# Performance work log

Measured on AMD Instinct MI355X. Metric: run time of the kernel, lower is better.

## Reference

```python
import jax, jax.numpy as jnp
import numpy as np

LS = (0, 2, 4, 6, 8)
L_IN, L_OUT, SYM = 8, 8, 2
A, B, N, C = 2, 2, 1024, 8  # ti_n, te_n, voxels, b_out

def _triples():
    out = []
    for l in range(0, L_OUT + 1, SYM):
        for l1 in range(0, L_IN + 1, SYM):
            for l2 in range(l1, L_IN + 1, SYM):
                if abs(l2 - l1) <= l <= l1 + l2:
                    out.append((l, l1, l2))
    return tuple(out)

TRIPLES = _triples()
# Clebsch-Gordan-like constants (fixed random; same structural shapes as the real CG tables)
_rng = np.random.RandomState(42)
CG_R = {t: jnp.asarray((_rng.randn(2 * t[0] + 1, 2 * t[1] + 1, 2 * t[2] + 1) * 0.1).astype(np.float32)) for t in TRIPLES}
CG_L = {t: jnp.asarray((_rng.randn(2 * t[0] + 1, 2 * t[2] + 1, 2 * t[1] + 1) * 0.1).astype(np.float32)) for t in TRIPLES}


def setup_inputs() -> dict:
    key = jax.random.key(0)
    ks = jax.random.split(key, 11)
    inp = {}
    for i, l in enumerate(LS):
        i_l = 5 if l == 0 else 2
        inp[f"x{l}"] = jax.random.normal(ks[i], (A, B, N, i_l, 2 * l + 1), dtype=jnp.float32)
        inp[f"w{l}"] = jax.random.uniform(ks[5 + i], (A, B, i_l, C, 2 * l + 1), dtype=jnp.float32) * 0.1
    inp["bias"] = jnp.zeros((A, B, 1, C, 1, 1), dtype=jnp.float32)
    return inp


def _forward(x0, x2, x4, x6, x8, w0, w2, w4, w6, w8, bias):
    xs = {0: x0, 2: x2, 4: x4, 6: x6, 8: x8}
    ws = {0: w0, 2: w2, 4: w4, 6: w6, 8: w8}
    # spectral convolution: rh[l] = x[l] @ w[l], shape (a,b,n,c,2l+1,2l+1)
    rh = {}
    for l in LS:
        r = jnp.einsum('abnil,abiok->abnolk', xs[l], ws[l])
        if l == 0:
            r = r + bias
        rh[l] = r
    # CG tensor-product quadratic nonlinearity
    rh_n = {}
    for (l, l1, l2) in TRIPLES:
        a, b, n, c = rh[l1].shape[:4]
        xx = jnp.einsum('abncij,klj->abnckli', rh[l2], CG_R[(l, l1, l2)])
        xx = xx.reshape(a, b, n, c, 2 * l + 1, -1)  # flat dim = (2l1+1)*(2l2+1)
        yy = jnp.einsum('abncji,klj->abnckil', rh[l1], CG_L[(l, l1, l2)])
        yy = yy.reshape(a, b, n, c, 2 * l + 1, -1)
        z = jnp.einsum('abncki,abncji->abnckj', yy, xx)  # (a,b,n,c,2l+1,2l+1)
        rh_n[l] = z if l not in rh_n else rh_n[l] + z
    # power-spectrum features
    feats = []
    for l in LS:
        n_l = np.float32(8.0 * np.pi ** 2 / (2 * l + 1))
        f = jnp.sum(rh_n[l] ** 2, axis=(4, 5)).reshape(A, B, -1)  # (a,b,n*c)
        feats.append(n_l * f)
    feats = jnp.concatenate(feats, axis=2)  # (a,b, 5*n*c)
    return feats, rh_n


def reference(x0, x2, x4, x6, x8, w0, w2, w4, w6, w8, bias):
    feats, rh_n = _forward(x0, x2, x4, x6, x8, w0, w2, w4, w6, w8, bias)
    return (feats, rh_n[0], rh_n[2], rh_n[4], rh_n[6], rh_n[8])
```

## Files before the change

kernel.cpp:

```cpp
#include <hip/hip_runtime.h>
#include <cmath>
#include <cstdint>
#include <vector>
#include <cstdlib>
#include <algorithm>

#define WGB 256

typedef float vf4 __attribute__((ext_vector_type(4)));

struct TripleMeta { int l,l1,l2,d,d1,d2,form,dp4,cgR,cgL,uvV,uvU; };
struct AllMeta { TripleMeta t[48]; int nT, cgTotal, uvTotal, uvUTotal; };

constexpr AllMeta build_meta() {
  AllMeta M{};
  const int LSl[5] = {0,2,4,6,8};
  int k=0, cg=0;
  for (int a=0;a<5;a++){ const int l=LSl[a];
    for (int b=0;b<5;b++){ const int l1=LSl[b];
      for (int l2=l1;l2<=8;l2+=2){
        if (!((l2-l1)<=l && l<=(l1+l2))) continue;
        TripleMeta m{};
        m.l=l; m.l1=l1; m.l2=l2;
        m.d=2*l+1; m.d1=2*l1+1; m.d2=2*l2+1;
        m.form = (l1==0) ? ((l2==0)?2:1) : 0;
        m.dp4 = ((m.d+3)/4)*4;
        m.cgR = cg; cg += m.d*m.d1*m.d2;
        M.t[k] = m; k++;
      } } }
  M.nT=k; M.cgTotal=cg;
  int cgl=cg;
  for (int i=0;i<k;i++){ M.t[i].cgL=cgl; cgl += M.t[i].d*M.t[i].d1*M.t[i].d2; }
  int uv=0, uvu=0;
  for (int i=0;i<k;i++){
    if (M.t[i].form==0){ M.t[i].uvV=uv; uv += 4*M.t[i].dp4; M.t[i].uvU=uvu; uvu += 4*M.t[i].d; }
    else if (M.t[i].form==1){ M.t[i].uvV=uv; uv += 2*M.t[i].dp4; M.t[i].uvU=uvu; uvu += 2*M.t[i].d + 2; }
  }
  M.uvTotal=uv; M.uvUTotal=uvu;
  return M;
}

constexpr AllMeta META_H = build_meta();
static_assert(META_H.nT==42, "nT");
static_assert(META_H.cgTotal==52334, "cgTotal");
static_assert(META_H.uvTotal==2048, "uvTotal");
static_assert(META_H.uvUTotal==1588, "uvUTotal");

__device__ constexpr AllMeta META = build_meta();

constexpr int CG_TOTAL  = 52334;
constexpr int UVS       = 2048;
constexpr int UVSU      = 1588;
constexpr int ZTOT      = 4520;
constexpr int XBS       = 104;
constexpr int WI_N      = 512;

constexpr int UOFF  = 4520;
constexpr int ROFF  = UOFF + 2*UVSU;
constexpr int FOFF  = ROFF + 16;
constexpr int SHTOT = FOFF + 360;

__device__ constexpr int DL[5]     = {1,5,9,13,17};
__device__ constexpr int T0G[6]    = {0,5,13,23,33,42};
__device__ constexpr int RHNB[5]   = {163840,196608,1015808,3670016,9207808};
__device__ constexpr int CBASE[5]  = {352,312,240,136,0};
__device__ constexpr int LEN5[5]   = {8,200,648,1352,2312};
__device__ constexpr int ZB[5]     = {0,8,208,856,2208};
__device__ constexpr int C4[6]     = {0,2,52,214,552,1130};

__device__ constexpr int SCHEDV[4][3][3] = {
  {{4,  0, 46},{2,  0, 36},{-1,0,0}},
  {{4, 46, 91},{2, 36, 72},{-1,0,0}},
  {{4, 91,136},{1,  0, 40},{ 0,0,8}},
  {{3,  0, 52},{3, 52,104},{-1,0,0}},
};

__global__ __launch_bounds__(128) void s2_prep(
    const float* __restrict__ w2, const float* __restrict__ w4,
    const float* __restrict__ w6, const float* __restrict__ w8,
    const float* __restrict__ cg, float* __restrict__ V)
{
  __shared__ float Rs[4928];
  const int bid = blockIdx.x;
  const int t   = bid >> 5;
  const int abc = bid & 31;
  const auto &m = META.t[t];
  if (m.form == 2) return;
  const int ab = abc >> 3, c = abc & 7;
  const int sz = m.d * m.d1 * m.d2;
  for (int i = threadIdx.x; i < sz; i += 128) Rs[i] = cg[m.cgR + i];
  __syncthreads();
  const float* ws[4] = {w2,w4,w6,w8};
  const int nout = (m.form==0 ? 4 : 2) * m.d;
  if ((int)threadIdx.x < nout){
    const int pq = threadIdx.x / m.d;
    const int k2 = threadIdx.x - pq*m.d;
    float s = 0.f;
    if (m.form==0){
      const int p = pq>>1, q = pq&1;
      const float* wA = ws[(m.l1>>1)-1] + ((ab*2+p)*8 + c)*m.d1;
      const float* wB = ws[(m.l2>>1)-1] + ((ab*2+q)*8 + c)*m.d2;
      const float* Rk = Rs + k2*m.d1*m.d2;
      for (int a=0;a<m.d1;a++){
        float t2 = 0.f;
        for (int j=0;j<m.d2;j++) t2 += wB[j]*Rk[a*m.d2+j];
        s += wA[a]*t2;
      }
    } else {
      const float* wB = ws[(m.l2>>1)-1] + ((ab*2+pq)*8 + c)*m.d2;
      const float* Rk = Rs + k2*m.d2;
      for (int j=0;j<m.d2;j++) s += wB[j]*Rk[j];
    }
    V[abc*UVS + m.uvV + pq*m.dp4 + k2] = s;
  }
}

template<int D1>
__device__ __forceinline__ void u_itemA(const float* __restrict__ Lp, const float* xb,
    float* Ush, int dst, int dstr, int xo1, int xo2, int d2)
{
  float x0r[2*D1], x1r[2*D1];
  #pragma unroll
  for (int j=0;j<2*D1;j++){ x0r[j] = xb[xo1+j]; x1r[j] = xb[XBS+xo1+j]; }
  float a00=0.f,a01=0.f,a10=0.f,a11=0.f;
  float b00=0.f,b01=0.f,b10=0.f,b11=0.f;
  for (int b=0;b<d2;b++){
    float i00=0.f, i01=0.f, i10=0.f, i11=0.f;
    const float* Lb = Lp + b*D1;
    #pragma unroll
    for (int j=0;j<D1;j++){
      const float lv=Lb[j];
      i00+=lv*x0r[j]; i01+=lv*x0r[D1+j];
      i10+=lv*x1r[j]; i11+=lv*x1r[D1+j];
    }
    const float q00=xb[xo2+b],     q01=xb[xo2+d2+b];
    const float q10=xb[XBS+xo2+b], q11=xb[XBS+xo2+d2+b];
    a00+=q00*i00; a01+=q01*i00; a10+=q00*i01; a11+=q01*i01;
    b00+=q10*i10; b01+=q11*i10; b10+=q10*i11; b11+=q11*i11;
  }
  Ush[dst]=a00; Ush[dst+dstr]=a01; Ush[dst+2*dstr]=a10; Ush[dst+3*dstr]=a11;
  Ush[UVSU+dst]=b00; Ush[UVSU+dst+dstr]=b01; Ush[UVSU+dst+2*dstr]=b10; Ush[UVSU+dst+3*dstr]=b11;
}

__device__ __forceinline__ void u_item(const int4 w, const float* __restrict__ cg,
                                       const float* xb, float* Ush)
{
  if (w.z == 0) return;
  const float* Lp = cg + w.x;
  const int dst = w.y & 0xFFFF, dstr = ((unsigned)w.y) >> 16;
  const int xo1 = w.z & 0xFF, xo2 = (w.z>>8)&0xFF;
  const int d1 = (w.z>>16)&0x3F, d2 = ((unsigned)w.z)>>22;
  if (d1 == 0){
    float a0=0.f, a1=0.f, b0=0.f, b1=0.f;
    for (int b=0;b<d2;b++){
      const float lv=Lp[b];
      a0+=lv*xb[xo2+b];     a1+=lv*xb[xo2+d2+b];
      b0+=lv*xb[XBS+xo2+b]; b1+=lv*xb[XBS+xo2+d2+b];
    }
    Ush[dst]=a0; Ush[dst+dstr]=a1;
    Ush[UVSU+dst]=b0; Ush[UVSU+dst+dstr]=b1;
    return;
  }
  switch(d1){
    case 5:  u_itemA<5>(Lp,xb,Ush,dst,dstr,xo1,xo2,d2); break;
    case 9:  u_itemA<9>(Lp,xb,Ush,dst,dstr,xo1,xo2,d2); break;
    case 13: u_itemA<13>(Lp,xb,Ush,dst,dstr,xo1,xo2,d2); break;
    default: u_itemA<17>(Lp,xb,Ush,dst,dstr,xo1,xo2,d2); break;
  }
}

template<int LI>
__device__ __forceinline__ float col_work(int k2, float rh0c, float c000,
    const float* __restrict__ Vc, const float* Ush_v,
    float* zsh, int zb)
{
  constexpr int d = 4*LI + 1;
  float za[d];
  #pragma unroll
  for (int i=0;i<d;i++) za[i] = 0.f;
  #pragma unroll
  for (int t=T0G[LI]; t<T0G[LI+1]; t++){
    const auto &m = META.t[t];
    if (m.form==2){
      za[0] += rh0c*rh0c*c000;
    } else if (m.form==1){
      const float v0 = Vc[m.uvV + k2] * rh0c;
      const float v1 = Vc[m.uvV + m.dp4 + k2] * rh0c;
      const float2* Up = reinterpret_cast<const float2*>(Ush_v + m.uvU);
      #pragma unroll
      for (int k1=0;k1<d;k1++){
        const float2 u = Up[k1];
        za[k1] += u.x*v0 + u.y*v1;
      }
    } else {
      const float v0 = Vc[m.uvV + k2];
      const float v1 = Vc[m.uvV + m.dp4 + k2];
      const float v2 = Vc[m.uvV + 2*m.dp4 + k2];
      const float v3 = Vc[m.uvV + 3*m.dp4 + k2];
      const float4* Up = reinterpret_cast<const float4*>(Ush_v + m.uvU);
      #pragma unroll
      for (int k1=0;k1<d;k1++){
        const float4 u = Up[k1];
        za[k1] += u.x*v0 + u.y*v1 + u.z*v2 + u.w*v3;
      }
    }
  }
  float s = 0.f;
  #pragma unroll
  for (int k1=0;k1<d;k1++){
    zsh[zb + k1*d + k2] = za[k1];
    s += za[k1]*za[k1];
  }
  return s;
}

template<int LI>
__device__ __forceinline__ void do_passv(int base, int end, int lane, int v,
    const float* __restrict__ Vab, const float* Ush, const float* rh0s,
    float* zsh, float* fpart, float c000)
{
  constexpr int d = 4*LI + 1;
  const int col = base + lane;
  if (col >= end) return;
  const int c  = col / d;
  const int k2 = col - c*d;
  const float s = col_work<LI>(k2, rh0s[v*8+c], c000, Vab + c*UVS, Ush + v*UVSU,
                               zsh, ZB[LI] + c*d*d);
  fpart[CBASE[LI] + col] = s;
}

__global__ __launch_bounds__(WGB,4) void s2_main(
    const float* __restrict__ x0, const float* __restrict__ x2, const float* __restrict__ x4,
    const float* __restrict__ x6, const float* __restrict__ x8,
    const float* __restrict__ w0, const float* __restrict__ bias,
    const float* __restrict__ cg, const int4* __restrict__ wiU,
    const float* __restrict__ V, float* __restrict__ out, float c000)
{
  __shared__ alignas(16) float SH[SHTOT];
  float* const xb    = SH;
  float* const Ush   = SH + UOFF;
  float* const rh0s  = SH + ROFF;
  float* const fpart = SH + FOFF;
  const int tid = threadIdx.x;
  const int bid = blockIdx.x;
  const int ab  = bid >> 9;

  {
    const int v  = tid >> 7;
    const int t2 = tid & 127;
    const int vox = bid*2 + v;
    float* xv = xb + v*XBS;
    if (t2 < 5)        xv[t2]           = x0[vox*5  + t2];
    else if (t2 < 15)  xv[8  + (t2-5)]  = x2[vox*10 + (t2-5)];
    else if (t2 < 33)  xv[18 + (t2-15)] = x4[vox*18 + (t2-15)];
    else if (t2 < 59)  xv[36 + (t2-33)] = x6[vox*26 + (t2-33)];
    else if (t2 < 93)  xv[62 + (t2-59)] = x8[vox*34 + (t2-59)];
    else if (t2 >= 96 && t2 < 104) {
      const int c = t2 - 96;
      float s = bias[ab*8 + c];
      for (int i=0;i<5;i++) s += x0[vox*5+i] * w0[(ab*5+i)*8 + c];
      rh0s[v*8 + c] = s;
    }
  }
  __syncthreads();

  #pragma unroll 1
  for (int it=0; it<2; it++) u_item(wiU[it*WGB + tid], cg, xb, Ush);
  __syncthreads();

  const float* Vab = V + (ab*8)*UVS;
  const int wid = tid>>6, lane = tid&63;
  #pragma unroll 1
  for (int v=0; v<2; v++){
    const int bid2 = bid*2 + v;
    #pragma unroll 1
    for (int pi=0; pi<3; pi++){
      const int li = SCHEDV[wid][pi][0];
      if (li < 0) break;
      const int base = SCHEDV[wid][pi][1], end = SCHEDV[wid][pi][2];
      switch(li){
        case 4:  do_passv<4>(base,end,lane,v,Vab,Ush,rh0s,SH,fpart,c000); break;
        case 3:  do_passv<3>(base,end,lane,v,Vab,Ush,rh0s,SH,fpart,c000); break;
        case 2:  do_passv<2>(base,end,lane,v,Vab,Ush,rh0s,SH,fpart,c000); break;
        case 1:  do_passv<1>(base,end,lane,v,Vab,Ush,rh0s,SH,fpart,c000); break;
        default: do_passv<0>(base,end,lane,v,Vab,Ush,rh0s,SH,fpart,c000); break;
      }
    }
    __syncthreads();

    for (int i4 = tid; i4 < 1130; i4 += WGB){
      int li;
      if      (i4 < C4[1]) li = 0;
      else if (i4 < C4[2]) li = 1;
      else if (i4 < C4[3]) li = 2;
      else if (i4 < C4[4]) li = 3;
      else                 li = 4;
      const int r4 = i4 - C4[li];
      const vf4 zv = *reinterpret_cast<const vf4*>(SH + ZB[li] + 4*r4);
      __builtin_nontemporal_store(zv, reinterpret_cast<vf4*>(out + RHNB[li] + bid2*LEN5[li] + 4*r4));
    }

    if (tid < 40){
      const int li = tid >> 3, c = tid & 7;
      const int d = DL[li];
      float s = 0.f;
      for (int k2=0;k2<d;k2++) s += fpart[CBASE[li] + c*d + k2];
      const double nl_d = 8.0*3.14159265358979323846*3.14159265358979323846/(double)(2*(2*li)+1);
      const int n = bid2 & 1023;
      __builtin_nontemporal_store((float)nl_d * s, out + ab*40960 + li*8192 + n*8 + c);
    }
    if (v==0) __syncthreads();
  }
}

namespace {

struct MTRng {
  uint32_t mt[624]; int mti;
  bool has_g; double g;
  void seed(uint32_t s){
    for (int pos=0; pos<624; pos++){ mt[pos]=s; s = 1812433253u*(s^(s>>30)) + (uint32_t)pos + 1u; }
    mti = 624; has_g=false; g=0.0;
  }
  uint32_t next32(){
    if (mti >= 624){
      for (int i=0;i<624;i++){
        uint32_t y = (mt[i]&0x80000000u) | (mt[(i+1)%624]&0x7fffffffu);
        mt[i] = mt[(i+397)%624] ^ (y>>1) ^ ((y&1u) ? 0x9908b0dfu : 0u);
      }
      mti = 0;
    }
    uint32_t y = mt[mti++];
    y ^= y>>11; y ^= (y<<7)&0x9d2c5680u; y ^= (y<<15)&0xefc60000u; y ^= y>>18;
    return y;
  }
  double rk_double(){
    uint32_t a = next32()>>5, b = next32()>>6;
    return (a*67108864.0 + b)/9007199254740992.0;
  }
  double gauss(){
    if (has_g){ has_g=false; return g; }
    double f,x1,x2,r2;
    do {
      x1 = 2.0*rk_double()-1.0;
      x2 = 2.0*rk_double()-1.0;
      r2 = x1*x1 + x2*x2;
    } while (r2 >= 1.0 || r2 == 0.0);
    f = std::sqrt(-2.0*std::log(r2)/r2);
    g = f*x1; has_g = true;
    return f*x2;
  }
};

constexpr int XOFS_H[5] = {0,8,18,36,62};

struct DeviceSetup {
  float* d_cg  = nullptr;
  float* d_v   = nullptr;
  int4*  d_wiU = nullptr;
  float  c000  = 0.f;
  DeviceSetup(){
    std::vector<float> h(2*CG_TOTAL);
    MTRng r; r.seed(42u);
    for (int i=0;i<2*CG_TOTAL;i++) h[i] = (float)(r.gauss()*0.1);
    c000 = h[META_H.t[0].cgL] * h[META_H.t[0].cgR];

    struct HItem { int d2; int4 e; };
    std::vector<HItem> grp[5];
    for (int t=0;t<META_H.nT;t++){
      const TripleMeta &m = META_H.t[t];
      if (m.form==0){
        const int xo1 = XOFS_H[m.l1>>1], xo2 = XOFS_H[m.l2>>1];
        for (int k1=0;k1<m.d;k1++){
          int4 e;
          e.x = m.cgL + k1*m.d1*m.d2;
          e.y = (m.uvU + k1*4) | (1<<16);
          e.z = xo1 | (xo2<<8) | (m.d1<<16) | (m.d2<<22);
          e.w = 0;
          grp[(m.l1>>1)-1].push_back({m.d2, e});
        }
      } else if (m.form==1){
        const int xo2 = XOFS_H[m.l2>>1];
        for (int k1=0;k1<m.d;k1++){
          int4 e;
          e.x = m.cgL + k1*m.d2;
          e.y = (m.uvU + k1*2) | (1<<16);
          e.z = (xo2<<8) | (0<<16) | (m.d2<<22);
          e.w = 0;
          grp[4].push_back({m.d2, e});
        }
      }
    }
    if (grp[0].size()!=111 || grp[1].size()!=128 || grp[2].size()!=89 ||
        grp[3].size()!=45  || grp[4].size()!=44) std::abort();
    for (int g=0; g<5; g++)
      std::stable_sort(grp[g].begin(), grp[g].end(),
                       [](const HItem&a, const HItem&b){ return a.d2 > b.d2; });

    int4 zero; zero.x=0; zero.y=0; zero.z=0; zero.w=0;
    std::vector<int4> wiU(WI_N, zero);
    auto place = [&](int iter, int w, const std::vector<HItem>& g, int s, int n){
      for (int i=0;i<n;i++) wiU[iter*256 + w*64 + i] = g[s+i].e;
    };
    place(0,0,grp[3],0,45);
    place(0,1,grp[2],0,64);
    place(0,2,grp[2],64,25);
    place(0,3,grp[1],0,64);
    place(1,0,grp[4],0,44);
    place(1,1,grp[0],64,47);
    place(1,2,grp[1],64,64);
    place(1,3,grp[0],0,64);

    (void)hipMalloc((void**)&d_cg,  sizeof(float)*2*CG_TOTAL);
    (void)hipMalloc((void**)&d_v,   sizeof(float)*32*UVS);
    (void)hipMalloc((void**)&d_wiU, sizeof(int4)*WI_N);
    (void)hipMemcpy(d_cg,  h.data(),    sizeof(float)*2*CG_TOTAL, hipMemcpyHostToDevice);
    (void)hipMemcpy(d_wiU, wiU.data(),  sizeof(int4)*WI_N,  hipMemcpyHostToDevice);
  }
};
DeviceSetup g_dev;

}

extern "C" void kernel_launch(void* const* d_in, const int* in_sizes, int n_in,
                              void* d_out, int out_size, void* d_ws, size_t ws_size,
                              hipStream_t stream)
{
  (void)in_sizes; (void)n_in; (void)d_ws; (void)ws_size; (void)out_size;
  const float* x0   = (const float*)d_in[0];
  const float* w0   = (const float*)d_in[1];
  const float* x2   = (const float*)d_in[2];
  const float* w2   = (const float*)d_in[3];
  const float* x4   = (const float*)d_in[4];
  const float* w4   = (const float*)d_in[5];
  const float* x6   = (const float*)d_in[6];
  const float* w6   = (const float*)d_in[7];
  const float* x8   = (const float*)d_in[8];
  const float* w8   = (const float*)d_in[9];
  const float* bias = (const float*)d_in[10];
  float* out = (float*)d_out;

  s2_prep<<<dim3(42*32), dim3(128), 0, stream>>>(w2,w4,w6,w8, g_dev.d_cg, g_dev.d_v);
  s2_main<<<dim3(2048), dim3(WGB), 0, stream>>>(x0,x2,x4,x6,x8, w0, bias,
                                                g_dev.d_cg, g_dev.d_wiU,
                                                g_dev.d_v, out, g_dev.c000);
}
```

Baseline: 227.8 us.

## Process one voxel per workgroup instead of two, reduce features via shared atomics

The main kernel now handles a single voxel per 256-thread workgroup and launches twice as many workgroups. The U-stage work items drop the second voxel's accumulators, and the loop over two voxels goes away. Shared memory shrinks, which may allow more resident workgroups. Per-column power-spectrum partials are now summed with shared-memory atomicAdd into 40 slots instead of a separate reduction pass. The cost is that per-workgroup overhead and the loads of the CG table and V are no longer amortised over two voxels.

```diff
diff --git a/kernel.cpp b/kernel.cpp
--- a/kernel.cpp
+++ b/kernel.cpp
@@ -56,14 +56,13 @@
 constexpr int WI_N      = 512;
 
 constexpr int UOFF  = 4520;
-constexpr int ROFF  = UOFF + 2*UVSU;
-constexpr int FOFF  = ROFF + 16;
-constexpr int SHTOT = FOFF + 360;
+constexpr int ROFF  = UOFF + UVSU;
+constexpr int FOFF  = ROFF + 8;
+constexpr int SHTOT = FOFF + 40;
 
 __device__ constexpr int DL[5]     = {1,5,9,13,17};
 __device__ constexpr int T0G[6]    = {0,5,13,23,33,42};
 __device__ constexpr int RHNB[5]   = {163840,196608,1015808,3670016,9207808};
-__device__ constexpr int CBASE[5]  = {352,312,240,136,0};
 __device__ constexpr int LEN5[5]   = {8,200,648,1352,2312};
 __device__ constexpr int ZB[5]     = {0,8,208,856,2208};
 __device__ constexpr int C4[6]     = {0,2,52,214,552,1130};
@@ -117,29 +116,24 @@
 
 template<int D1>
 __device__ __forceinline__ void u_itemA(const float* __restrict__ Lp, const float* xb,
-    float* Ush, int dst, int dstr, int xo1, int xo2, int d2)
-{
-  float x0r[2*D1], x1r[2*D1];
+    float* Ush, int dst, int xo1, int xo2, int d2)
+{
+  float x0r[2*D1];
   #pragma unroll
-  for (int j=0;j<2*D1;j++){ x0r[j] = xb[xo1+j]; x1r[j] = xb[XBS+xo1+j]; }
+  for (int j=0;j<2*D1;j++) x0r[j] = xb[xo1+j];
   float a00=0.f,a01=0.f,a10=0.f,a11=0.f;
-  float b00=0.f,b01=0.f,b10=0.f,b11=0.f;
   for (int b=0;b<d2;b++){
-    float i00=0.f, i01=0.f, i10=0.f, i11=0.f;
+    float i0=0.f, i1=0.f;
     const float* Lb = Lp + b*D1;
     #pragma unroll
     for (int j=0;j<D1;j++){
       const float lv=Lb[j];
-      i00+=lv*x0r[j]; i01+=lv*x0r[D1+j];
-      i10+=lv*x1r[j]; i11+=lv*x1r[D1+j];
-    }
-    const float q00=xb[xo2+b],     q01=xb[xo2+d2+b];
-    const float q10=xb[XBS+xo2+b], q11=xb[XBS+xo2+d2+b];
-    a00+=q00*i00; a01+=q01*i00; a10+=q00*i01; a11+=q01*i01;
-    b00+=q10*i10; b01+=q11*i10; b10+=q10*i11; b11+=q11*i11;
-  }
-  Ush[dst]=a00; Ush[dst+dstr]=a01; Ush[dst+2*dstr]=a10; Ush[dst+3*dstr]=a11;
-  Ush[UVSU+dst]=b00; Ush[UVSU+dst+dstr]=b01; Ush[UVSU+dst+2*dstr]=b10; Ush[UVSU+dst+3*dstr]=b11;
+      i0+=lv*x0r[j]; i1+=lv*x0r[D1+j];
+    }
+    const float q0=xb[xo2+b], q1=xb[xo2+d2+b];
+    a00+=q0*i0; a01+=q1*i0; a10+=q0*i1; a11+=q1*i1;
+  }
+  Ush[dst]=a00; Ush[dst+1]=a01; Ush[dst+2]=a10; Ush[dst+3]=a11;
 }
 
 __device__ __forceinline__ void u_item(const int4 w, const float* __restrict__ cg,
@@ -147,25 +141,23 @@
 {
   if (w.z == 0) return;
   const float* Lp = cg + w.x;
-  const int dst = w.y & 0xFFFF, dstr = ((unsigned)w.y) >> 16;
+  const int dst = w.y & 0xFFFF;
   const int xo1 = w.z & 0xFF, xo2 = (w.z>>8)&0xFF;
   const int d1 = (w.z>>16)&0x3F, d2 = ((unsigned)w.z)>>22;
   if (d1 == 0){
-    float a0=0.f, a1=0.f, b0=0.f, b1=0.f;
+    float a0=0.f, a1=0.f;
     for (int b=0;b<d2;b++){
       const float lv=Lp[b];
-      a0+=lv*xb[xo2+b];     a1+=lv*xb[xo2+d2+b];
-      b0+=lv*xb[XBS+xo2+b]; b1+=lv*xb[XBS+xo2+d2+b];
-    }
-    Ush[dst]=a0; Ush[dst+dstr]=a1;
-    Ush[UVSU+dst]=b0; Ush[UVSU+dst+dstr]=b1;
+      a0+=lv*xb[xo2+b]; a1+=lv*xb[xo2+d2+b];
+    }
+    Ush[dst]=a0; Ush[dst+1]=a1;
     return;
   }
   switch(d1){
-    case 5:  u_itemA<5>(Lp,xb,Ush,dst,dstr,xo1,xo2,d2); break;
-    case 9:  u_itemA<9>(Lp,xb,Ush,dst,dstr,xo1,xo2,d2); break;
-    case 13: u_itemA<13>(Lp,xb,Ush,dst,dstr,xo1,xo2,d2); break;
-    default: u_itemA<17>(Lp,xb,Ush,dst,dstr,xo1,xo2,d2); break;
+    case 5:  u_itemA<5>(Lp,xb,Ush,dst,xo1,xo2,d2); break;
+    case 9:  u_itemA<9>(Lp,xb,Ush,dst,xo1,xo2,d2); break;
+    case 13: u_itemA<13>(Lp,xb,Ush,dst,xo1,xo2,d2); break;
+    default: u_itemA<17>(Lp,xb,Ush,dst,xo1,xo2,d2); break;
   }
 }
 
@@ -215,7 +207,7 @@
 }
 
 template<int LI>
-__device__ __forceinline__ void do_passv(int base, int end, int lane, int v,
+__device__ __forceinline__ void do_passv(int base, int end, int lane,
     const float* __restrict__ Vab, const float* Ush, const float* rh0s,
     float* zsh, float* fpart, float c000)
 {
@@ -224,9 +216,9 @@
   if (col >= end) return;
   const int c  = col / d;
   const int k2 = col - c*d;
-  const float s = col_work<LI>(k2, rh0s[v*8+c], c000, Vab + c*UVS, Ush + v*UVSU,
+  const float s = col_work<LI>(k2, rh0s[c], c000, Vab + c*UVS, Ush,
                                zsh, ZB[LI] + c*d*d);
-  fpart[CBASE[LI] + col] = s;
+  atomicAdd(fpart + LI*8 + c, s);
 }
 
 __global__ __launch_bounds__(WGB,4) void s2_main(
@@ -243,23 +235,22 @@
   float* const fpart = SH + FOFF;
   const int tid = threadIdx.x;
   const int bid = blockIdx.x;
-  const int ab  = bid >> 9;
-
+  const int ab  = bid >> 10;
+
+  if (tid < 40) fpart[tid] = 0.f;
   {
-    const int v  = tid >> 7;
-    const int t2 = tid & 127;
-    const int vox = bid*2 + v;
-    float* xv = xb + v*XBS;
-    if (t2 < 5)        xv[t2]           = x0[vox*5  + t2];
-    else if (t2 < 15)  xv[8  + (t2-5)]  = x2[vox*10 + (t2-5)];
-    else if (t2 < 33)  xv[18 + (t2-15)] = x4[vox*18 + (t2-15)];
-    else if (t2 < 59)  xv[36 + (t2-33)] = x6[vox*26 + (t2-33)];
-    else if (t2 < 93)  xv[62 + (t2-59)] = x8[vox*34 + (t2-59)];
+    const int t2 = tid;
+    const int vox = bid;
+    if (t2 < 5)        xb[t2]           = x0[vox*5  + t2];
+    else if (t2 < 15)  xb[8  + (t2-5)]  = x2[vox*10 + (t2-5)];
+    else if (t2 < 33)  xb[18 + (t2-15)] = x4[vox*18 + (t2-15)];
+    else if (t2 < 59)  xb[36 + (t2-33)] = x6[vox*26 + (t2-33)];
+    else if (t2 < 93)  xb[62 + (t2-59)] = x8[vox*34 + (t2-59)];
     else if (t2 >= 96 && t2 < 104) {
       const int c = t2 - 96;
       float s = bias[ab*8 + c];
       for (int i=0;i<5;i++) s += x0[vox*5+i] * w0[(ab*5+i)*8 + c];
-      rh0s[v*8 + c] = s;
+      rh0s[c] = s;
     }
   }
   __syncthreads();
@@ -271,45 +262,37 @@
   const float* Vab = V + (ab*8)*UVS;
   const int wid = tid>>6, lane = tid&63;
   #pragma unroll 1
-  for (int v=0; v<2; v++){
-    const int bid2 = bid*2 + v;
-    #pragma unroll 1
-    for (int pi=0; pi<3; pi++){
-      const int li = SCHEDV[wid][pi][0];
-      if (li < 0) break;
-      const int base = SCHEDV[wid][pi][1], end = SCHEDV[wid][pi][2];
-      switch(li){
-        case 4:  do_passv<4>(base,end,lane,v,Vab,Ush,rh0s,SH,fpart,c000); break;
-        case 3:  do_passv<3>(base,end,lane,v,Vab,Ush,rh0s,SH,fpart,c000); break;
-        case 2:  do_passv<2>(base,end,lane,v,Vab,Ush,rh0s,SH,fpart,c000); break;
-        case 1:  do_passv<1>(base,end,lane,v,Vab,Ush,rh0s,SH,fpart,c000); break;
-        default: do_passv<0>(base,end,lane,v,Vab,Ush,rh0s,SH,fpart,c000); break;
-      }
-    }
-    __syncthreads();
-
-    for (int i4 = tid; i4 < 1130; i4 += WGB){
-      int li;
-      if      (i4 < C4[1]) li = 0;
-      else if (i4 < C4[2]) li = 1;
-      else if (i4 < C4[3]) li = 2;
-      else if (i4 < C4[4]) li = 3;
-      else                 li = 4;
-      const int r4 = i4 - C4[li];
-      const vf4 zv = *reinterpret_cast<const vf4*>(SH + ZB[li] + 4*r4);
-      __builtin_nontemporal_store(zv, reinterpret_cast<vf4*>(out + RHNB[li] + bid2*LEN5[li] + 4*r4));
-    }
-
-    if (tid < 40){
-      const int li = tid >> 3, c = tid & 7;
-      const int d = DL[li];
-      float s = 0.f;
-      for (int k2=0;k2<d;k2++) s += fpart[CBASE[li] + c*d + k2];
-      const double nl_d = 8.0*3.14159265358979323846*3.14159265358979323846/(double)(2*(2*li)+1);
-      const int n = bid2 & 1023;
-      __builtin_nontemporal_store((float)nl_d * s, out + ab*40960 + li*8192 + n*8 + c);
-    }
-    if (v==0) __syncthreads();
+  for (int pi=0; pi<3; pi++){
+    const int li = SCHEDV[wid][pi][0];
+    if (li < 0) break;
+    const int base = SCHEDV[wid][pi][1], end = SCHEDV[wid][pi][2];
+    switch(li){
+      case 4:  do_passv<4>(base,end,lane,Vab,Ush,rh0s,SH,fpart,c000); break;
+      case 3:  do_passv<3>(base,end,lane,Vab,Ush,rh0s,SH,fpart,c000); break;
+      case 2:  do_passv<2>(base,end,lane,Vab,Ush,rh0s,SH,fpart,c000); break;
+      case 1:  do_passv<1>(base,end,lane,Vab,Ush,rh0s,SH,fpart,c000); break;
+      default: do_passv<0>(base,end,lane,Vab,Ush,rh0s,SH,fpart,c000); break;
+    }
+  }
+  __syncthreads();
+
+  for (int i4 = tid; i4 < 1130; i4 += WGB){
+    int li;
+    if      (i4 < C4[1]) li = 0;
+    else if (i4 < C4[2]) li = 1;
+    else if (i4 < C4[3]) li = 2;
+    else if (i4 < C4[4]) li = 3;
+    else                 li = 4;
+    const int r4 = i4 - C4[li];
+    const vf4 zv = *reinterpret_cast<const vf4*>(SH + ZB[li] + 4*r4);
+    __builtin_nontemporal_store(zv, reinterpret_cast<vf4*>(out + RHNB[li] + bid*LEN5[li] + 4*r4));
+  }
+
+  if (tid < 40){
+    const int li = tid >> 3, c = tid & 7;
+    const double nl_d = 8.0*3.14159265358979323846*3.14159265358979323846/(double)(2*(2*li)+1);
+    const int n = bid & 1023;
+    __builtin_nontemporal_store((float)nl_d * fpart[tid], out + ab*40960 + li*8192 + n*8 + c);
   }
 }
 
@@ -374,7 +357,7 @@
         for (int k1=0;k1<m.d;k1++){
           int4 e;
           e.x = m.cgL + k1*m.d1*m.d2;
-          e.y = (m.uvU + k1*4) | (1<<16);
+          e.y = (m.uvU + k1*4);
           e.z = xo1 | (xo2<<8) | (m.d1<<16) | (m.d2<<22);
           e.w = 0;
           grp[(m.l1>>1)-1].push_back({m.d2, e});
@@ -384,7 +367,7 @@
         for (int k1=0;k1<m.d;k1++){
           int4 e;
           e.x = m.cgL + k1*m.d2;
-          e.y = (m.uvU + k1*2) | (1<<16);
+          e.y = (m.uvU + k1*2);
           e.z = (xo2<<8) | (0<<16) | (m.d2<<22);
           e.w = 0;
           grp[4].push_back({m.d2, e});
@@ -441,7 +424,7 @@
   float* out = (float*)d_out;
 
   s2_prep<<<dim3(42*32), dim3(128), 0, stream>>>(w2,w4,w6,w8, g_dev.d_cg, g_dev.d_v);
-  s2_main<<<dim3(2048), dim3(WGB), 0, stream>>>(x0,x2,x4,x6,x8, w0, bias,
+  s2_main<<<dim3(4096), dim3(WGB), 0, stream>>>(x0,x2,x4,x6,x8, w0, bias,
                                                 g_dev.d_cg, g_dev.d_wiU,
                                                 g_dev.d_v, out, g_dev.c000);
 }
```

Result: slower. 260.2 us (+14.2%).
